# Kernel tuning notes

Measured on AMD Instinct MI355X. Metric: run time of the kernel, lower is better.

The kernel has to match this reference:

```python
import jax, jax.numpy as jnp
import numpy as np

USER = 50000
ITEM = 50000
LATDIM = 128
N_LAYERS = 3
N_NODES = USER + ITEM
N_EDGES = 1600000


def setup_inputs() -> dict:
    key = jax.random.key(0)
    k1, k2, k3, k4, k5 = jax.random.split(key, 5)
    uEmbeds = jax.random.normal(k1, (USER, LATDIM), dtype=jnp.float32)
    iEmbeds = jax.random.normal(k2, (ITEM, LATDIM), dtype=jnp.float32)
    edge_src = jax.random.randint(k3, (N_EDGES,), 0, N_NODES, dtype=jnp.int32)
    edge_dst = jax.random.randint(k4, (N_EDGES,), 0, N_NODES, dtype=jnp.int32)
    edge_val = jax.random.uniform(k5, (N_EDGES,), dtype=jnp.float32)
    return {"uEmbeds": uEmbeds, "iEmbeds": iEmbeds,
            "edge_src": edge_src, "edge_dst": edge_dst, "edge_val": edge_val}


def _spmm(edge_src, edge_dst, edge_val, embeds):
    # sparse [N,N] @ dense [N,D]: gather rows at src, scale, scatter-add at dst
    msg = embeds[edge_src] * edge_val[:, None]  # [E, D]
    return jax.ops.segment_sum(msg, edge_dst, num_segments=N_NODES)


def reference(uEmbeds, iEmbeds, edge_src, edge_dst, edge_val):
    embeds = jnp.concatenate([uEmbeds, iEmbeds], axis=0)  # [N, D]
    acc = embeds
    cur = embeds
    for _ in range(N_LAYERS):
        cur = _spmm(edge_src, edge_dst, edge_val, cur)
        acc = acc + cur
    return acc[:USER], acc[USER:]
```

## Files before the change

### kernel.cpp

```cpp
#include <hip/hip_runtime.h>


static constexpr int USERS  = 50000;
static constexpr int NNODES = 100000;
static constexpr int DIM    = 128;
static constexpr int NEDGES = 1600000;
static constexpr long NELEM = (long)NNODES * DIM;
static constexpr int NBK    = (NNODES + 255) / 256;
static constexpr int EPW    = 4096;
static constexpr int NWG    = (NEDGES + EPW - 1) / EPW;
static constexpr int SSROW  = NBK + 1;
static constexpr int INITB  = (int)((NELEM / 16 + 255) / 256);

__device__ __forceinline__ unsigned short f2bf(float f) {
    unsigned int u = __float_as_uint(f);
    unsigned int r = (u + 0x7FFFu + ((u >> 16) & 1)) >> 16;
    return (unsigned short)r;
}
__device__ __forceinline__ unsigned int pack2(float a, float b) {
    return (unsigned int)f2bf(a) | ((unsigned int)f2bf(b) << 16);
}
__device__ __forceinline__ float bflo(unsigned int p) { return __uint_as_float(p << 16); }
__device__ __forceinline__ float bfhi(unsigned int p) { return __uint_as_float(p & 0xFFFF0000u); }

__global__ void __launch_bounds__(256) initpart_k(
    const float* __restrict__ uE, const float* __restrict__ iE,
    const int* __restrict__ esrc, const int* __restrict__ edst,
    const float* __restrict__ eval,
    unsigned int* __restrict__ E0, int* __restrict__ ssP,
    int* __restrict__ gcnt, int2* __restrict__ tmp) {
    __shared__ int2 stage[EPW];
    __shared__ int hist[NBK];
    __shared__ int cursor[NBK];
    __shared__ int sp[256];
    int t = threadIdx.x;

    if (blockIdx.x >= NWG) {
        long base = ((long)(blockIdx.x - NWG) * 256 + t) * 16;
        if (base >= NELEM) return;
        const long usplit = (long)USERS * DIM;
        const float* s = (base < usplit) ? (uE + base) : (iE + (base - usplit));
        #pragma unroll
        for (int h = 0; h < 2; ++h) {
            float4 f0 = *(const float4*)(s + h * 8);
            float4 f1 = *(const float4*)(s + h * 8 + 4);
            uint4 o;
            o.x = pack2(f0.x, f0.y); o.y = pack2(f0.z, f0.w);
            o.z = pack2(f1.x, f1.y); o.w = pack2(f1.z, f1.w);
            *(uint4*)(E0 + base / 2 + h * 4) = o;
        }
        return;
    }

    int w = blockIdx.x;
    int ebase = w * EPW;
    int n = NEDGES - ebase; if (n > EPW) n = EPW;

    for (int b = t; b < NBK; b += 256) hist[b] = 0;
    __syncthreads();
    #pragma unroll
    for (int k = 0; k < EPW / 256; ++k) {
        int idx = k * 256 + t;
        if (idx < n) atomicAdd(&hist[edst[ebase + idx] >> 8], 1);
    }
    __syncthreads();
    for (int b = t; b < NBK; b += 256)
        if (hist[b]) atomicAdd(&gcnt[b], hist[b]);
    int b0 = 2 * t, b1 = 2 * t + 1;
    int v0 = (b0 < NBK) ? hist[b0] : 0;
    int v1 = (b1 < NBK) ? hist[b1] : 0;
    int psum = v0 + v1;
    sp[t] = psum;
    __syncthreads();
    for (int o = 1; o < 256; o <<= 1) {
        int x = (t >= o) ? sp[t - o] : 0;
        __syncthreads();
        sp[t] += x;
        __syncthreads();
    }
    int pref = sp[t] - psum;
    if (b0 < NBK) cursor[b0] = pref;
    if (b1 < NBK) cursor[b1] = pref + v0;
    __syncthreads();
    for (int b = t; b < NBK; b += 256) ssP[w * SSROW + b] = cursor[b];
    if (t == 0) ssP[w * SSROW + NBK] = n;
    __syncthreads();
    #pragma unroll
    for (int k = 0; k < EPW / 256; ++k) {
        int idx = k * 256 + t;
        if (idx < n) {
            int e = ebase + idx;
            int d = edst[e];
            int p = atomicAdd(&cursor[d >> 8], 1);
            stage[p] = make_int2(esrc[e] | ((d & 255) << 17), __float_as_int(eval[e]));
        }
    }
    __syncthreads();
    #pragma unroll
    for (int k = 0; k < EPW / 256; ++k) {
        int idx = k * 256 + t;
        if (idx < n) tmp[ebase + idx] = stage[idx];
    }
}

__global__ void __launch_bounds__(256) fill2_k(
    const int2* __restrict__ tmp, const int* __restrict__ ssP,
    const int* __restrict__ gcnt,
    int* __restrict__ rs, unsigned int* __restrict__ meta) {
    __shared__ int cnt[256];
    __shared__ int cur[256];
    __shared__ int sp2[256];
    __shared__ int sbase;
    int b = blockIdx.x, t = threadIdx.x;
    int b0 = 2 * t, b1 = 2 * t + 1;
    int g0 = (b0 < NBK) ? gcnt[b0] : 0;
    int g1 = (b1 < NBK) ? gcnt[b1] : 0;
    int ps = g0 + g1;
    sp2[t] = ps;
    __syncthreads();
    for (int o = 1; o < 256; o <<= 1) {
        int x = (t >= o) ? sp2[t - o] : 0;
        __syncthreads();
        sp2[t] += x;
        __syncthreads();
    }
    int pref = sp2[t] - ps;
    if (b0 == b) sbase = pref;
    if (b1 == b) sbase = pref + g0;
    if (b == 0 && t == 0) rs[NNODES] = NEDGES;
    cnt[t] = 0;
    __syncthreads();
    int base = sbase;
    for (int w = t; w < NWG; w += 256) {
        int s = ssP[w * SSROW + b];
        int e = ssP[w * SSROW + b + 1];
        const int2* seg = tmp + (long)w * EPW;
        for (int i = s; i < e; ++i)
            atomicAdd(&cnt[(seg[i].x >> 17) & 255], 1);
    }
    __syncthreads();
    int myc = cnt[t];
    sp2[t] = myc;
    __syncthreads();
    for (int o = 1; o < 256; o <<= 1) {
        int x = (t >= o) ? sp2[t - o] : 0;
        __syncthreads();
        sp2[t] += x;
        __syncthreads();
    }
    int start = base + sp2[t] - myc;
    int node = b * 256 + t;
    if (node < NNODES) rs[node] = start;
    cur[t] = start;
    __syncthreads();
    for (int w = t; w < NWG; w += 256) {
        int s = ssP[w * SSROW + b];
        int e = ssP[w * SSROW + b + 1];
        const int2* seg = tmp + (long)w * EPW;
        for (int i = s; i < e; ++i) {
            int2 m = seg[i];
            int slot = atomicAdd(&cur[(m.x >> 17) & 255], 1);
            unsigned int bv = (unsigned int)(f2bf(__int_as_float(m.y)) & 0x7FFF);
            meta[slot] = (unsigned int)(m.x & 0x1FFFF) | (bv << 17);
        }
    }
}

__device__ __forceinline__ void gather_row(
    const unsigned int* __restrict__ meta, const unsigned int* __restrict__ cur,
    int beg, int end, int lane, float& outx, float& outy) {
    float accx[8], accy[8];
    #pragma unroll
    for (int k = 0; k < 8; ++k) { accx[k] = 0.f; accy[k] = 0.f; }
    int i = beg;
    for (; i + 8 <= end; i += 8) {
        unsigned int m[8], p[8];
        #pragma unroll
        for (int k = 0; k < 8; ++k) m[k] = __builtin_nontemporal_load(&meta[i + k]);
        #pragma unroll
        for (int k = 0; k < 8; ++k) p[k] = cur[((m[k] & 0x1FFFF) << 6) + lane];
        #pragma unroll
        for (int k = 0; k < 8; ++k) {
            float v = __uint_as_float((m[k] >> 17) << 16);
            accx[k] += bflo(p[k]) * v;
            accy[k] += bfhi(p[k]) * v;
        }
    }
    if (i + 4 <= end) {
        unsigned int m[4], p[4];
        #pragma unroll
        for (int k = 0; k < 4; ++k) m[k] = __builtin_nontemporal_load(&meta[i + k]);
        #pragma unroll
        for (int k = 0; k < 4; ++k) p[k] = cur[((m[k] & 0x1FFFF) << 6) + lane];
        #pragma unroll
        for (int k = 0; k < 4; ++k) {
            float v = __uint_as_float((m[k] >> 17) << 16);
            accx[k] += bflo(p[k]) * v;
            accy[k] += bfhi(p[k]) * v;
        }
        i += 4;
    }
    for (; i < end; ++i) {
        unsigned int m = __builtin_nontemporal_load(&meta[i]);
        unsigned int p = cur[((m & 0x1FFFF) << 6) + lane];
        float v = __uint_as_float((m >> 17) << 16);
        accx[0] += bflo(p) * v;
        accy[0] += bfhi(p) * v;
    }
    outx = ((accx[0] + accx[1]) + (accx[2] + accx[3]))
         + ((accx[4] + accx[5]) + (accx[6] + accx[7]));
    outy = ((accy[0] + accy[1]) + (accy[2] + accy[3]))
         + ((accy[4] + accy[5]) + (accy[6] + accy[7]));
}

__global__ void __launch_bounds__(256) gather_k(
    const int* __restrict__ rs, const unsigned int* __restrict__ meta,
    const unsigned int* __restrict__ cur, unsigned int* __restrict__ nxt) {
    int row = blockIdx.x * 4 + (threadIdx.x >> 6);
    if (row >= NNODES) return;
    int lane = threadIdx.x & 63;
    float sx, sy;
    gather_row(meta, cur, rs[row], rs[row + 1], lane, sx, sy);
    nxt[(row << 6) + lane] = pack2(sx, sy);
}

__global__ void __launch_bounds__(256) gather_last_k(
    const int* __restrict__ rs, const unsigned int* __restrict__ meta,
    const unsigned int* __restrict__ cur,
    const unsigned int* __restrict__ L1,
    const unsigned int* __restrict__ E0,
    float* __restrict__ out) {
    int row = blockIdx.x * 4 + (threadIdx.x >> 6);
    if (row >= NNODES) return;
    int lane = threadIdx.x & 63;
    float sx, sy;
    gather_row(meta, cur, rs[row], rs[row + 1], lane, sx, sy);
    unsigned int e0 = E0[(row << 6) + lane];
    unsigned int l1 = L1[(row << 6) + lane];
    unsigned int l2 = cur[(row << 6) + lane];
    float2 o;
    o.x = bflo(e0) + bflo(l1) + bflo(l2) + sx;
    o.y = bfhi(e0) + bfhi(l1) + bfhi(l2) + sy;
    *(float2*)(out + (long)row * DIM + lane * 2) = o;
}

__global__ void init_f32_k(const float* __restrict__ uE, const float* __restrict__ iE,
                           float* __restrict__ acc, float* __restrict__ cur) {
    long base = ((long)blockIdx.x * blockDim.x + threadIdx.x) * 8;
    if (base >= NELEM) return;
    const long usplit = (long)USERS * DIM;
    const float* s = (base < usplit) ? (uE + base) : (iE + (base - usplit));
    float4 f0 = *(const float4*)(s);
    float4 f1 = *(const float4*)(s + 4);
    *(float4*)(acc + base)     = f0;
    *(float4*)(acc + base + 4) = f1;
    *(float4*)(cur + base)     = f0;
    *(float4*)(cur + base + 4) = f1;
}
__global__ void scatter_k(const int* __restrict__ esrc, const int* __restrict__ edst,
                          const float* __restrict__ eval,
                          const float* __restrict__ cur, float* __restrict__ nxt) {
    long g = (long)blockIdx.x * blockDim.x + threadIdx.x;
    if (g >= (long)NEDGES * 32) return;
    int e  = (int)(g >> 5);
    int d0 = ((int)g & 31) * 4;
    float v = eval[e];
    float4 x = *(const float4*)(cur + (long)esrc[e] * DIM + d0);
    float* o = nxt + (long)edst[e] * DIM + d0;
    unsafeAtomicAdd(o + 0, x.x * v);
    unsafeAtomicAdd(o + 1, x.y * v);
    unsafeAtomicAdd(o + 2, x.z * v);
    unsafeAtomicAdd(o + 3, x.w * v);
}
__global__ void add_k(float* __restrict__ acc, const float* __restrict__ nxt) {
    long g = ((long)blockIdx.x * blockDim.x + threadIdx.x) * 4;
    if (g >= NELEM) return;
    float4 a = *(const float4*)(acc + g);
    float4 n = *(const float4*)(nxt + g);
    a.x += n.x; a.y += n.y; a.z += n.z; a.w += n.w;
    *(float4*)(acc + g) = a;
}

extern "C" void kernel_launch(void* const* d_in, const int* in_sizes, int n_in,
                              void* d_out, int out_size, void* d_ws, size_t ws_size,
                              hipStream_t stream) {
    const float* uE   = (const float*)d_in[0];
    const float* iE   = (const float*)d_in[1];
    const int*   esrc = (const int*)d_in[2];
    const int*   edst = (const int*)d_in[3];
    const float* eval = (const float*)d_in[4];
    float* out = (float*)d_out;

    char* ws = (char*)d_ws;
    const long NU = NELEM / 2;
    unsigned int* E0  = (unsigned int*)ws;
    unsigned int* L1  = E0 + NU;
    unsigned int* L2b = L1 + NU;
    unsigned int* meta = (unsigned int*)(L2b + NU);
    int*  rs     = (int*)(meta + NEDGES);
    int*  gcnt   = rs + NNODES + 1;
    int*  ssP    = gcnt + NBK;
    size_t need  = (size_t)((char*)(ssP + NWG * SSROW) - ws);
    int2* tmp = (int2*)L2b;

    if (ws_size >= need) {
        hipMemsetAsync(gcnt, 0, (size_t)NBK * sizeof(int), stream);
        initpart_k<<<NWG + INITB, 256, 0, stream>>>(uE, iE, esrc, edst, eval,
                                                    E0, ssP, gcnt, tmp);
        fill2_k<<<NBK, 256, 0, stream>>>(tmp, ssP, gcnt, rs, meta);

        const int gblocks = (NNODES + 3) / 4;
        gather_k<<<gblocks, 256, 0, stream>>>(rs, meta, E0, L1);
        gather_k<<<gblocks, 256, 0, stream>>>(rs, meta, L1, L2b);
        gather_last_k<<<gblocks, 256, 0, stream>>>(rs, meta, L2b, L1, E0, out);
    } else {
        float* bufA = (float*)ws;
        float* bufB = bufA + NELEM;
        const size_t SZ = (size_t)NELEM * sizeof(float);
        init_f32_k<<<(int)((NELEM / 8 + 255) / 256), 256, 0, stream>>>(uE, iE, out, bufA);
        float* cur = bufA;
        float* nxt = bufB;
        for (int l = 0; l < 3; ++l) {
            hipMemsetAsync(nxt, 0, SZ, stream);
            long nthreads = (long)NEDGES * 32;
            scatter_k<<<(int)((nthreads + 255) / 256), 256, 0, stream>>>(esrc, edst, eval, cur, nxt);
            add_k<<<(int)((NELEM / 4 + 255) / 256), 256, 0, stream>>>(out, nxt);
            float* t = cur; cur = nxt; nxt = t;
        }
    }
}
```

Measured before the change: 295.9 us.

## Stage bucket edges in LDS for CSR fill; gather rows with half-wave uint2 loads

```diff
diff --git a/kernel.cpp b/kernel.cpp
--- a/kernel.cpp
+++ b/kernel.cpp
@@ -11,6 +11,7 @@
 static constexpr int NWG    = (NEDGES + EPW - 1) / EPW;
 static constexpr int SSROW  = NBK + 1;
 static constexpr int INITB  = (int)((NELEM / 16 + 255) / 256);
+static constexpr int SCAP   = 5120;
 
 __device__ __forceinline__ unsigned short f2bf(float f) {
     unsigned int u = __float_as_uint(f);
@@ -107,11 +108,13 @@
     const int2* __restrict__ tmp, const int* __restrict__ ssP,
     const int* __restrict__ gcnt,
     int* __restrict__ rs, unsigned int* __restrict__ meta) {
+    __shared__ int2 stage[SCAP];
     __shared__ int cnt[256];
     __shared__ int cur[256];
     __shared__ int sp2[256];
     __shared__ int sbase;
     int b = blockIdx.x, t = threadIdx.x;
+
     int b0 = 2 * t, b1 = 2 * t + 1;
     int g0 = (b0 < NBK) ? gcnt[b0] : 0;
     int g1 = (b1 < NBK) ? gcnt[b1] : 0;
@@ -128,19 +131,13 @@
     if (b0 == b) sbase = pref;
     if (b1 == b) sbase = pref + g0;
     if (b == 0 && t == 0) rs[NNODES] = NEDGES;
-    cnt[t] = 0;
     __syncthreads();
     int base = sbase;
-    for (int w = t; w < NWG; w += 256) {
-        int s = ssP[w * SSROW + b];
-        int e = ssP[w * SSROW + b + 1];
-        const int2* seg = tmp + (long)w * EPW;
-        for (int i = s; i < e; ++i)
-            atomicAdd(&cnt[(seg[i].x >> 17) & 255], 1);
-    }
-    __syncthreads();
-    int myc = cnt[t];
-    sp2[t] = myc;
+
+    int mylen = 0;
+    for (int w = t; w < NWG; w += 256)
+        mylen += ssP[w * SSROW + b + 1] - ssP[w * SSROW + b];
+    sp2[t] = mylen;
     __syncthreads();
     for (int o = 1; o < 256; o <<= 1) {
         int x = (t >= o) ? sp2[t - o] : 0;
@@ -148,100 +145,155 @@
         sp2[t] += x;
         __syncthreads();
     }
-    int start = base + sp2[t] - myc;
-    int node = b * 256 + t;
-    if (node < NNODES) rs[node] = start;
-    cur[t] = start;
-    __syncthreads();
-    for (int w = t; w < NWG; w += 256) {
-        int s = ssP[w * SSROW + b];
-        int e = ssP[w * SSROW + b + 1];
-        const int2* seg = tmp + (long)w * EPW;
-        for (int i = s; i < e; ++i) {
-            int2 m = seg[i];
+    int myoff = sp2[t] - mylen;
+    int nb = sp2[255];
+    __syncthreads();
+
+    if (nb <= SCAP) {
+        int o = myoff;
+        for (int w = t; w < NWG; w += 256) {
+            int s = ssP[w * SSROW + b];
+            int e = ssP[w * SSROW + b + 1];
+            const int2* seg = tmp + (long)w * EPW;
+            for (int i = s; i < e; ++i) stage[o++] = seg[i];
+        }
+        cnt[t] = 0;
+        __syncthreads();
+        for (int i = t; i < nb; i += 256)
+            atomicAdd(&cnt[(stage[i].x >> 17) & 255], 1);
+        __syncthreads();
+        int myc = cnt[t];
+        sp2[t] = myc;
+        __syncthreads();
+        for (int o2 = 1; o2 < 256; o2 <<= 1) {
+            int x = (t >= o2) ? sp2[t - o2] : 0;
+            __syncthreads();
+            sp2[t] += x;
+            __syncthreads();
+        }
+        int start = base + sp2[t] - myc;
+        int node = b * 256 + t;
+        if (node < NNODES) rs[node] = start;
+        cur[t] = start;
+        __syncthreads();
+        for (int i = t; i < nb; i += 256) {
+            int2 m = stage[i];
             int slot = atomicAdd(&cur[(m.x >> 17) & 255], 1);
             unsigned int bv = (unsigned int)(f2bf(__int_as_float(m.y)) & 0x7FFF);
             meta[slot] = (unsigned int)(m.x & 0x1FFFF) | (bv << 17);
         }
-    }
-}
-
-__device__ __forceinline__ void gather_row(
-    const unsigned int* __restrict__ meta, const unsigned int* __restrict__ cur,
-    int beg, int end, int lane, float& outx, float& outy) {
-    float accx[8], accy[8];
+    } else {
+        cnt[t] = 0;
+        __syncthreads();
+        for (int w = t; w < NWG; w += 256) {
+            int s = ssP[w * SSROW + b];
+            int e = ssP[w * SSROW + b + 1];
+            const int2* seg = tmp + (long)w * EPW;
+            for (int i = s; i < e; ++i)
+                atomicAdd(&cnt[(seg[i].x >> 17) & 255], 1);
+        }
+        __syncthreads();
+        int myc = cnt[t];
+        sp2[t] = myc;
+        __syncthreads();
+        for (int o2 = 1; o2 < 256; o2 <<= 1) {
+            int x = (t >= o2) ? sp2[t - o2] : 0;
+            __syncthreads();
+            sp2[t] += x;
+            __syncthreads();
+        }
+        int start = base + sp2[t] - myc;
+        int node = b * 256 + t;
+        if (node < NNODES) rs[node] = start;
+        cur[t] = start;
+        __syncthreads();
+        for (int w = t; w < NWG; w += 256) {
+            int s = ssP[w * SSROW + b];
+            int e = ssP[w * SSROW + b + 1];
+            const int2* seg = tmp + (long)w * EPW;
+            for (int i = s; i < e; ++i) {
+                int2 m = seg[i];
+                int slot = atomicAdd(&cur[(m.x >> 17) & 255], 1);
+                unsigned int bv = (unsigned int)(f2bf(__int_as_float(m.y)) & 0x7FFF);
+                meta[slot] = (unsigned int)(m.x & 0x1FFFF) | (bv << 17);
+            }
+        }
+    }
+}
+
+__device__ __forceinline__ void gather_row_u2(
+    const unsigned int* __restrict__ meta, const uint2* __restrict__ curU2,
+    int beg, int end, int sub, float& s0, float& s1, float& s2, float& s3) {
+    float a[4][4];
     #pragma unroll
-    for (int k = 0; k < 8; ++k) { accx[k] = 0.f; accy[k] = 0.f; }
+    for (int k = 0; k < 4; ++k)
+        #pragma unroll
+        for (int j = 0; j < 4; ++j) a[k][j] = 0.f;
     int i = beg;
-    for (; i + 8 <= end; i += 8) {
-        unsigned int m[8], p[8];
-        #pragma unroll
-        for (int k = 0; k < 8; ++k) m[k] = __builtin_nontemporal_load(&meta[i + k]);
-        #pragma unroll
-        for (int k = 0; k < 8; ++k) p[k] = cur[((m[k] & 0x1FFFF) << 6) + lane];
-        #pragma unroll
-        for (int k = 0; k < 8; ++k) {
-            float v = __uint_as_float((m[k] >> 17) << 16);
-            accx[k] += bflo(p[k]) * v;
-            accy[k] += bfhi(p[k]) * v;
-        }
-    }
-    if (i + 4 <= end) {
-        unsigned int m[4], p[4];
+    for (; i + 4 <= end; i += 4) {
+        unsigned int m[4];
+        uint2 p[4];
         #pragma unroll
         for (int k = 0; k < 4; ++k) m[k] = __builtin_nontemporal_load(&meta[i + k]);
         #pragma unroll
-        for (int k = 0; k < 4; ++k) p[k] = cur[((m[k] & 0x1FFFF) << 6) + lane];
+        for (int k = 0; k < 4; ++k) p[k] = curU2[((m[k] & 0x1FFFF) << 5) + sub];
         #pragma unroll
         for (int k = 0; k < 4; ++k) {
             float v = __uint_as_float((m[k] >> 17) << 16);
-            accx[k] += bflo(p[k]) * v;
-            accy[k] += bfhi(p[k]) * v;
-        }
-        i += 4;
+            a[k][0] += bflo(p[k].x) * v;
+            a[k][1] += bfhi(p[k].x) * v;
+            a[k][2] += bflo(p[k].y) * v;
+            a[k][3] += bfhi(p[k].y) * v;
+        }
     }
     for (; i < end; ++i) {
         unsigned int m = __builtin_nontemporal_load(&meta[i]);
-        unsigned int p = cur[((m & 0x1FFFF) << 6) + lane];
+        uint2 p = curU2[((m & 0x1FFFF) << 5) + sub];
         float v = __uint_as_float((m >> 17) << 16);
-        accx[0] += bflo(p) * v;
-        accy[0] += bfhi(p) * v;
-    }
-    outx = ((accx[0] + accx[1]) + (accx[2] + accx[3]))
-         + ((accx[4] + accx[5]) + (accx[6] + accx[7]));
-    outy = ((accy[0] + accy[1]) + (accy[2] + accy[3]))
-         + ((accy[4] + accy[5]) + (accy[6] + accy[7]));
+        a[0][0] += bflo(p.x) * v;
+        a[0][1] += bfhi(p.x) * v;
+        a[0][2] += bflo(p.y) * v;
+        a[0][3] += bfhi(p.y) * v;
+    }
+    s0 = (a[0][0] + a[1][0]) + (a[2][0] + a[3][0]);
+    s1 = (a[0][1] + a[1][1]) + (a[2][1] + a[3][1]);
+    s2 = (a[0][2] + a[1][2]) + (a[2][2] + a[3][2]);
+    s3 = (a[0][3] + a[1][3]) + (a[2][3] + a[3][3]);
 }
 
 __global__ void __launch_bounds__(256) gather_k(
     const int* __restrict__ rs, const unsigned int* __restrict__ meta,
-    const unsigned int* __restrict__ cur, unsigned int* __restrict__ nxt) {
-    int row = blockIdx.x * 4 + (threadIdx.x >> 6);
+    const uint2* __restrict__ cur, uint2* __restrict__ nxt) {
+    int lane = threadIdx.x & 63;
+    int row = blockIdx.x * 8 + (threadIdx.x >> 6) * 2 + (lane >> 5);
     if (row >= NNODES) return;
-    int lane = threadIdx.x & 63;
-    float sx, sy;
-    gather_row(meta, cur, rs[row], rs[row + 1], lane, sx, sy);
-    nxt[(row << 6) + lane] = pack2(sx, sy);
+    int sub = lane & 31;
+    float s0, s1, s2, s3;
+    gather_row_u2(meta, cur, rs[row], rs[row + 1], sub, s0, s1, s2, s3);
+    nxt[(row << 5) + sub] = make_uint2(pack2(s0, s1), pack2(s2, s3));
 }
 
 __global__ void __launch_bounds__(256) gather_last_k(
     const int* __restrict__ rs, const unsigned int* __restrict__ meta,
-    const unsigned int* __restrict__ cur,
-    const unsigned int* __restrict__ L1,
-    const unsigned int* __restrict__ E0,
+    const uint2* __restrict__ cur,
+    const uint2* __restrict__ L1,
+    const uint2* __restrict__ E0,
     float* __restrict__ out) {
-    int row = blockIdx.x * 4 + (threadIdx.x >> 6);
+    int lane = threadIdx.x & 63;
+    int row = blockIdx.x * 8 + (threadIdx.x >> 6) * 2 + (lane >> 5);
     if (row >= NNODES) return;
-    int lane = threadIdx.x & 63;
-    float sx, sy;
-    gather_row(meta, cur, rs[row], rs[row + 1], lane, sx, sy);
-    unsigned int e0 = E0[(row << 6) + lane];
-    unsigned int l1 = L1[(row << 6) + lane];
-    unsigned int l2 = cur[(row << 6) + lane];
-    float2 o;
-    o.x = bflo(e0) + bflo(l1) + bflo(l2) + sx;
-    o.y = bfhi(e0) + bfhi(l1) + bfhi(l2) + sy;
-    *(float2*)(out + (long)row * DIM + lane * 2) = o;
+    int sub = lane & 31;
+    float s0, s1, s2, s3;
+    gather_row_u2(meta, cur, rs[row], rs[row + 1], sub, s0, s1, s2, s3);
+    uint2 e0 = E0[(row << 5) + sub];
+    uint2 l1 = L1[(row << 5) + sub];
+    uint2 l2 = cur[(row << 5) + sub];
+    float4 o;
+    o.x = bflo(e0.x) + bflo(l1.x) + bflo(l2.x) + s0;
+    o.y = bfhi(e0.x) + bfhi(l1.x) + bfhi(l2.x) + s1;
+    o.z = bflo(e0.y) + bflo(l1.y) + bflo(l2.y) + s2;
+    o.w = bfhi(e0.y) + bfhi(l1.y) + bfhi(l2.y) + s3;
+    *(float4*)(out + (long)row * DIM + sub * 4) = o;
 }
 
 __global__ void init_f32_k(const float* __restrict__ uE, const float* __restrict__ iE,
@@ -309,10 +361,11 @@
                                                     E0, ssP, gcnt, tmp);
         fill2_k<<<NBK, 256, 0, stream>>>(tmp, ssP, gcnt, rs, meta);
 
-        const int gblocks = (NNODES + 3) / 4;
-        gather_k<<<gblocks, 256, 0, stream>>>(rs, meta, E0, L1);
-        gather_k<<<gblocks, 256, 0, stream>>>(rs, meta, L1, L2b);
-        gather_last_k<<<gblocks, 256, 0, stream>>>(rs, meta, L2b, L1, E0, out);
+        const int gblocks = (NNODES + 7) / 8;
+        gather_k<<<gblocks, 256, 0, stream>>>(rs, meta, (const uint2*)E0, (uint2*)L1);
+        gather_k<<<gblocks, 256, 0, stream>>>(rs, meta, (const uint2*)L1, (uint2*)L2b);
+        gather_last_k<<<gblocks, 256, 0, stream>>>(rs, meta, (const uint2*)L2b,
+                                                   (const uint2*)L1, (const uint2*)E0, out);
     } else {
         float* bufA = (float*)ws;
         float* bufB = bufA + NELEM;
```

Measured after the change: 276.6 us. -6.5%, faster.
